# Optimization experiments

Measured on AMD Instinct MI355X. Metric: run time of the kernel, lower is better.

## Reference

```python
import jax, jax.numpy as jnp
import numpy as np

N_NODES = 100000

def sage_conv(x, edge_index, Wl, bl, Wr):
    # PyG SAGEConv: out = lin_l(mean_agg(x_src -> dst)) + lin_r(x)
    src, dst = edge_index[0], edge_index[1]
    msgs = x[src]                                   # [E, F] gather
    sums = jax.ops.segment_sum(msgs, dst, num_segments=N_NODES)   # [N, F]
    cnt = jax.ops.segment_sum(jnp.ones((edge_index.shape[1],), x.dtype), dst,
                              num_segments=N_NODES)               # [N]
    mean = sums / jnp.maximum(cnt, 1.0)[:, None]
    return mean @ Wl + bl + x @ Wr


def setup_inputs() -> dict:
    key = jax.random.key(0)
    ks = jax.random.split(key, 12)
    in_dim, hid = 32, 64
    x = jax.random.normal(ks[0], (N_NODES, in_dim), dtype=jnp.float32)
    edge_index = jax.random.randint(ks[1], (2, 3200000), 0, N_NODES)
    edge_pairs = jax.random.randint(ks[2], (1000000, 2), 0, N_NODES)
    def lin(k, fi, fo):
        bound = 1.0 / np.sqrt(fi)
        return jax.random.uniform(k, (fi, fo), jnp.float32, -bound, bound)
    params = {
        'Wl1': lin(ks[3], in_dim, hid), 'bl1': jnp.zeros((hid,), jnp.float32),
        'Wr1': lin(ks[4], in_dim, hid),
        'Wl2': lin(ks[5], hid, hid),    'bl2': jnp.zeros((hid,), jnp.float32),
        'Wr2': lin(ks[6], hid, hid),
        'Wh':  lin(ks[7], 2 * hid, 1),  'bh': jnp.zeros((1,), jnp.float32),
    }
    return dict(x=x, edge_index=edge_index, edge_pairs=edge_pairs, **params)


def reference(x, edge_index, edge_pairs, Wl1, bl1, Wr1, Wl2, bl2, Wr2, Wh, bh):
    h = jax.nn.relu(sage_conv(x, edge_index, Wl1, bl1, Wr1))
    h = jax.nn.relu(sage_conv(h, edge_index, Wl2, bl2, Wr2))
    src = h[edge_pairs[:, 0]]
    dst = h[edge_pairs[:, 1]]
    edge_repr = jnp.concatenate([src, dst], axis=1)   # [P, 2*hid]
    logits = (edge_repr @ Wh + bh)[:, 0]              # [P]
    return logits
```

## Files before the change

kernel.cpp:

```cpp
#include <hip/hip_runtime.h>

typedef unsigned int uint;
typedef unsigned short ushort;
typedef __attribute__((ext_vector_type(8))) short bf16x8;
typedef __attribute__((ext_vector_type(4))) float f32x4;

#define N_NODES 100000
#define N_EDGES 3200000
#define N_PAIRS 1000000
#define N_TILES (N_NODES / 16)

#define BUCK_SHIFT 8
#define BUCK_NODES 256
#define NBUCK ((N_NODES + BUCK_NODES - 1) / BUCK_NODES)
#define CAP 8704
#define CH 2048
#define NCHB ((N_EDGES + CH - 1) / CH)
#define EPT (CH / 256)

__device__ __forceinline__ float bf_lo(uint u) { return __uint_as_float(u << 16); }
__device__ __forceinline__ float bf_hi(uint u) { return __uint_as_float(u & 0xFFFF0000u); }
__device__ __forceinline__ ushort f2bf(float f) {
  uint u = __float_as_uint(f);
  return (ushort)((u + 0x7FFF + ((u >> 16) & 1)) >> 16);
}
__device__ __forceinline__ uint pack2bf(float lo, float hi) {
  return (uint)f2bf(lo) | ((uint)f2bf(hi) << 16);
}


__global__ void __launch_bounds__(256) k_prep(
    const float* __restrict__ x,
    const float* __restrict__ Wl1, const float* __restrict__ Wr1,
    const float* __restrict__ Wl2, const float* __restrict__ Wr2,
    ushort* __restrict__ xb, ushort* __restrict__ W1T, ushort* __restrict__ W2T,
    int* __restrict__ woff)
{
  int t = blockIdx.x * blockDim.x + threadIdx.x;
  if (t < N_NODES * 32) xb[t] = f2bf(x[t]);
  if (t < 4096) {
    int col = t >> 6, f = t & 63;
    float w = (f < 32) ? Wl1[f * 64 + col] : Wr1[(f - 32) * 64 + col];
    W1T[col * 64 + f] = f2bf(w);
  }
  if (t < 8192) {
    int col = t >> 7, f = t & 127;
    float w = (f < 64) ? Wl2[f * 64 + col] : Wr2[(f - 64) * 64 + col];
    W2T[col * 128 + f] = f2bf(w);
  }
  if (t < NBUCK) woff[t] = t * CAP;
}


__global__ void __launch_bounds__(256) k_binning(
    const int* __restrict__ src, const int* __restrict__ dst,
    int* __restrict__ woff, int* __restrict__ bucket_data)
{
  __shared__ int hist[NBUCK];
  __shared__ int rbase[NBUCK];
  int t = threadIdx.x;
  int lo = blockIdx.x * CH;
  int hi = lo + CH; if (hi > N_EDGES) hi = N_EDGES;
  for (int i = t; i < NBUCK; i += 256) hist[i] = 0;
  __syncthreads();
  int d0 = -1, d1 = -1, d2 = -1, d3 = -1, d4 = -1, d5 = -1, d6 = -1, d7 = -1;
  int s0 = 0, s1 = 0, s2 = 0, s3 = 0, s4 = 0, s5 = 0, s6 = 0, s7 = 0;
#define LOADK(k, dk, sk)                                     \
  { int e = lo + t + k * 256;                                \
    if (e < hi) { dk = dst[e]; sk = src[e];                  \
                  atomicAdd(&hist[dk >> BUCK_SHIFT], 1); } }
  LOADK(0, d0, s0) LOADK(1, d1, s1) LOADK(2, d2, s2) LOADK(3, d3, s3)
  LOADK(4, d4, s4) LOADK(5, d5, s5) LOADK(6, d6, s6) LOADK(7, d7, s7)
#undef LOADK
  __syncthreads();
  for (int i = t; i < NBUCK; i += 256) {
    int h = hist[i];
    rbase[i] = h ? atomicAdd(&woff[i], h) : 0;
    hist[i] = 0;
  }
  __syncthreads();
#define STOREK(dk, sk)                                       \
  if (dk >= 0) {                                             \
    int b = dk >> BUCK_SHIFT;                                \
    int r = atomicAdd(&hist[b], 1);                          \
    int pos = rbase[b] + r;                                  \
    if (pos < (b + 1) * CAP)                                 \
      bucket_data[pos] = (sk << BUCK_SHIFT) | (dk & (BUCK_NODES - 1)); }
  STOREK(d0, s0) STOREK(d1, s1) STOREK(d2, s2) STOREK(d3, s3)
  STOREK(d4, s4) STOREK(d5, s5) STOREK(d6, s6) STOREK(d7, s7)
#undef STOREK
}


__global__ void __launch_bounds__(512) k_bucket_csr(
    const int* __restrict__ woff, const int* __restrict__ bucket_data,
    int* __restrict__ csr, int* __restrict__ row_beg, int* __restrict__ row_end)
{
  __shared__ int hist[BUCK_NODES];
  __shared__ int sc[BUCK_NODES];
  __shared__ int offs[BUCK_NODES];
  int b = blockIdx.x;
  int t = threadIdx.x;
  int base = b * CAP;
  int cnt = woff[b] - base;
  const int* bd = bucket_data + base;
  if (t < BUCK_NODES) hist[t] = 0;
  __syncthreads();
  for (int i = t; i < cnt; i += 512) atomicAdd(&hist[bd[i] & (BUCK_NODES - 1)], 1);
  __syncthreads();
  if (t < BUCK_NODES) sc[t] = hist[t];
  __syncthreads();
  for (int off = 1; off < BUCK_NODES; off <<= 1) {
    int u = 0;
    if (t < BUCK_NODES && t >= off) u = sc[t - off];
    __syncthreads();
    if (t < BUCK_NODES) sc[t] += u;
    __syncthreads();
  }
  if (t < BUCK_NODES) {
    int start = base + sc[t] - hist[t];
    offs[t] = start;
    int node = b * BUCK_NODES + t;
    if (node < N_NODES) { row_beg[node] = start; row_end[node] = start + hist[t]; }
  }
  __syncthreads();
  for (int i = t; i < cnt; i += 512) {
    int pv = bd[i];
    int pos = atomicAdd(&offs[pv & (BUCK_NODES - 1)], 1);
    csr[pos] = pv >> BUCK_SHIFT;
  }
}


__global__ void __launch_bounds__(256) k_gather1(
    const uint4* __restrict__ xb4, const int* __restrict__ row_beg,
    const int* __restrict__ row_end, const int* __restrict__ csr,
    uint4* __restrict__ mean1)
{
  int gid = blockIdx.x * blockDim.x + threadIdx.x;
  int n = gid >> 6;
  int lane = threadIdx.x & 63;
  if (n >= N_NODES) return;
  int slot = lane >> 2;
  int fq = lane & 3;
  int beg = row_beg[n], end = row_end[n];
  int deg = end - beg;
  float s0 = 0.f, s1 = 0.f, s2 = 0.f, s3 = 0.f, s4 = 0.f, s5 = 0.f, s6 = 0.f, s7 = 0.f;
  int i = beg;
  for (; i + 31 < end; i += 32) {
    int n0 = csr[i + slot];
    int n1 = csr[i + 16 + slot];
    uint4 a = xb4[n0 * 4 + fq];
    uint4 b = xb4[n1 * 4 + fq];
    s0 += bf_lo(a.x); s1 += bf_hi(a.x); s2 += bf_lo(a.y); s3 += bf_hi(a.y);
    s4 += bf_lo(a.z); s5 += bf_hi(a.z); s6 += bf_lo(a.w); s7 += bf_hi(a.w);
    s0 += bf_lo(b.x); s1 += bf_hi(b.x); s2 += bf_lo(b.y); s3 += bf_hi(b.y);
    s4 += bf_lo(b.z); s5 += bf_hi(b.z); s6 += bf_lo(b.w); s7 += bf_hi(b.w);
  }
  for (; i < end; i += 16) {
    if (i + slot < end) {
      uint4 a = xb4[csr[i + slot] * 4 + fq];
      s0 += bf_lo(a.x); s1 += bf_hi(a.x); s2 += bf_lo(a.y); s3 += bf_hi(a.y);
      s4 += bf_lo(a.z); s5 += bf_hi(a.z); s6 += bf_lo(a.w); s7 += bf_hi(a.w);
    }
  }
#pragma unroll
  for (int off = 4; off <= 32; off <<= 1) {
    s0 += __shfl_xor(s0, off); s1 += __shfl_xor(s1, off);
    s2 += __shfl_xor(s2, off); s3 += __shfl_xor(s3, off);
    s4 += __shfl_xor(s4, off); s5 += __shfl_xor(s5, off);
    s6 += __shfl_xor(s6, off); s7 += __shfl_xor(s7, off);
  }
  if (slot == 0) {
    float invd = (deg > 0) ? 1.f / (float)deg : 0.f;
    uint4 o;
    o.x = pack2bf(s0 * invd, s1 * invd);
    o.y = pack2bf(s2 * invd, s3 * invd);
    o.z = pack2bf(s4 * invd, s5 * invd);
    o.w = pack2bf(s6 * invd, s7 * invd);
    mean1[n * 4 + fq] = o;
  }
}

__global__ void __launch_bounds__(256) k_gather2(
    const uint4* __restrict__ hb4, const int* __restrict__ row_beg,
    const int* __restrict__ row_end, const int* __restrict__ csr,
    uint4* __restrict__ mean2)
{
  int gid = blockIdx.x * blockDim.x + threadIdx.x;
  int n = gid >> 6;
  int lane = threadIdx.x & 63;
  if (n >= N_NODES) return;
  int slot = lane >> 3;
  int fq = lane & 7;
  int beg = row_beg[n], end = row_end[n];
  int deg = end - beg;
  float s0 = 0.f, s1 = 0.f, s2 = 0.f, s3 = 0.f, s4 = 0.f, s5 = 0.f, s6 = 0.f, s7 = 0.f;
  int i = beg;
  for (; i + 31 < end; i += 32) {
    int n0 = csr[i + slot];
    int n1 = csr[i + 8 + slot];
    int n2 = csr[i + 16 + slot];
    int n3 = csr[i + 24 + slot];
    uint4 a = hb4[n0 * 8 + fq];
    uint4 b = hb4[n1 * 8 + fq];
    uint4 c = hb4[n2 * 8 + fq];
    uint4 d = hb4[n3 * 8 + fq];
    s0 += bf_lo(a.x); s1 += bf_hi(a.x); s2 += bf_lo(a.y); s3 += bf_hi(a.y);
    s4 += bf_lo(a.z); s5 += bf_hi(a.z); s6 += bf_lo(a.w); s7 += bf_hi(a.w);
    s0 += bf_lo(b.x); s1 += bf_hi(b.x); s2 += bf_lo(b.y); s3 += bf_hi(b.y);
    s4 += bf_lo(b.z); s5 += bf_hi(b.z); s6 += bf_lo(b.w); s7 += bf_hi(b.w);
    s0 += bf_lo(c.x); s1 += bf_hi(c.x); s2 += bf_lo(c.y); s3 += bf_hi(c.y);
    s4 += bf_lo(c.z); s5 += bf_hi(c.z); s6 += bf_lo(c.w); s7 += bf_hi(c.w);
    s0 += bf_lo(d.x); s1 += bf_hi(d.x); s2 += bf_lo(d.y); s3 += bf_hi(d.y);
    s4 += bf_lo(d.z); s5 += bf_hi(d.z); s6 += bf_lo(d.w); s7 += bf_hi(d.w);
  }
  for (; i < end; i += 8) {
    if (i + slot < end) {
      uint4 a = hb4[csr[i + slot] * 8 + fq];
      s0 += bf_lo(a.x); s1 += bf_hi(a.x); s2 += bf_lo(a.y); s3 += bf_hi(a.y);
      s4 += bf_lo(a.z); s5 += bf_hi(a.z); s6 += bf_lo(a.w); s7 += bf_hi(a.w);
    }
  }
#pragma unroll
  for (int off = 8; off <= 32; off <<= 1) {
    s0 += __shfl_xor(s0, off); s1 += __shfl_xor(s1, off);
    s2 += __shfl_xor(s2, off); s3 += __shfl_xor(s3, off);
    s4 += __shfl_xor(s4, off); s5 += __shfl_xor(s5, off);
    s6 += __shfl_xor(s6, off); s7 += __shfl_xor(s7, off);
  }
  if (slot == 0) {
    float invd = (deg > 0) ? 1.f / (float)deg : 0.f;
    uint4 o;
    o.x = pack2bf(s0 * invd, s1 * invd);
    o.y = pack2bf(s2 * invd, s3 * invd);
    o.z = pack2bf(s4 * invd, s5 * invd);
    o.w = pack2bf(s6 * invd, s7 * invd);
    mean2[n * 8 + fq] = o;
  }
}


__global__ void __launch_bounds__(256) k_gemm1(
    const ushort* __restrict__ mean1, const ushort* __restrict__ xb,
    const ushort* __restrict__ W1T, const float* __restrict__ bl,
    ushort* __restrict__ h1b)
{
  int wave = (blockIdx.x * blockDim.x + threadIdx.x) >> 6;
  if (wave >= N_TILES) return;
  int lane = threadIdx.x & 63;
  int lc = lane & 15;
  int lg = lane >> 4;
  int n0 = wave * 16;

  bf16x8 bfr[4][2];
#pragma unroll
  for (int j = 0; j < 4; ++j)
#pragma unroll
    for (int kk = 0; kk < 2; ++kk)
      bfr[j][kk] = *(const bf16x8*)(W1T + (j * 16 + lc) * 64 + kk * 32 + lg * 8);

  f32x4 c[4];
#pragma unroll
  for (int j = 0; j < 4; ++j) {
    float b = bl[j * 16 + lc];
    c[j][0] = b; c[j][1] = b; c[j][2] = b; c[j][3] = b;
  }

  bf16x8 a0 = *(const bf16x8*)(mean1 + (n0 + lc) * 32 + lg * 8);
  bf16x8 a1 = *(const bf16x8*)(xb    + (n0 + lc) * 32 + lg * 8);
#pragma unroll
  for (int j = 0; j < 4; ++j) {
    c[j] = __builtin_amdgcn_mfma_f32_16x16x32_bf16(a0, bfr[j][0], c[j], 0, 0, 0);
    c[j] = __builtin_amdgcn_mfma_f32_16x16x32_bf16(a1, bfr[j][1], c[j], 0, 0, 0);
  }

#pragma unroll
  for (int j = 0; j < 4; ++j)
#pragma unroll
    for (int r = 0; r < 4; ++r) {
      int node = n0 + lg * 4 + r;
      h1b[node * 64 + j * 16 + lc] = f2bf(fmaxf(c[j][r], 0.f));
    }
}

__global__ void __launch_bounds__(256) k_gemm2(
    const ushort* __restrict__ mean2, const ushort* __restrict__ h1b,
    const ushort* __restrict__ W2T, const float* __restrict__ bl,
    const float* __restrict__ Wh, float* __restrict__ u, float* __restrict__ v)
{
  int wave = (blockIdx.x * blockDim.x + threadIdx.x) >> 6;
  if (wave >= N_TILES) return;
  int lane = threadIdx.x & 63;
  int lc = lane & 15;
  int lg = lane >> 4;
  int n0 = wave * 16;

  bf16x8 bfr[4][4];
#pragma unroll
  for (int j = 0; j < 4; ++j)
#pragma unroll
    for (int kk = 0; kk < 4; ++kk)
      bfr[j][kk] = *(const bf16x8*)(W2T + (j * 16 + lc) * 128 + kk * 32 + lg * 8);

  f32x4 c[4];
#pragma unroll
  for (int j = 0; j < 4; ++j) {
    float b = bl[j * 16 + lc];
    c[j][0] = b; c[j][1] = b; c[j][2] = b; c[j][3] = b;
  }

  bf16x8 a0 = *(const bf16x8*)(mean2 + (n0 + lc) * 64 + lg * 8);
  bf16x8 a1 = *(const bf16x8*)(mean2 + (n0 + lc) * 64 + 32 + lg * 8);
  bf16x8 a2 = *(const bf16x8*)(h1b   + (n0 + lc) * 64 + lg * 8);
  bf16x8 a3 = *(const bf16x8*)(h1b   + (n0 + lc) * 64 + 32 + lg * 8);
#pragma unroll
  for (int j = 0; j < 4; ++j) {
    c[j] = __builtin_amdgcn_mfma_f32_16x16x32_bf16(a0, bfr[j][0], c[j], 0, 0, 0);
    c[j] = __builtin_amdgcn_mfma_f32_16x16x32_bf16(a1, bfr[j][1], c[j], 0, 0, 0);
    c[j] = __builtin_amdgcn_mfma_f32_16x16x32_bf16(a2, bfr[j][2], c[j], 0, 0, 0);
    c[j] = __builtin_amdgcn_mfma_f32_16x16x32_bf16(a3, bfr[j][3], c[j], 0, 0, 0);
  }

  float pu0 = 0.f, pu1 = 0.f, pu2 = 0.f, pu3 = 0.f;
  float pv0 = 0.f, pv1 = 0.f, pv2 = 0.f, pv3 = 0.f;
#pragma unroll
  for (int j = 0; j < 4; ++j) {
    float wu = Wh[j * 16 + lc];
    float wv = Wh[64 + j * 16 + lc];
    float r0 = fmaxf(c[j][0], 0.f), r1 = fmaxf(c[j][1], 0.f);
    float r2 = fmaxf(c[j][2], 0.f), r3 = fmaxf(c[j][3], 0.f);
    pu0 = fmaf(r0, wu, pu0); pv0 = fmaf(r0, wv, pv0);
    pu1 = fmaf(r1, wu, pu1); pv1 = fmaf(r1, wv, pv1);
    pu2 = fmaf(r2, wu, pu2); pv2 = fmaf(r2, wv, pv2);
    pu3 = fmaf(r3, wu, pu3); pv3 = fmaf(r3, wv, pv3);
  }
#pragma unroll
  for (int off = 1; off <= 8; off <<= 1) {
    pu0 += __shfl_xor(pu0, off); pv0 += __shfl_xor(pv0, off);
    pu1 += __shfl_xor(pu1, off); pv1 += __shfl_xor(pv1, off);
    pu2 += __shfl_xor(pu2, off); pv2 += __shfl_xor(pv2, off);
    pu3 += __shfl_xor(pu3, off); pv3 += __shfl_xor(pv3, off);
  }
  if (lc == 0) {
    int node = n0 + lg * 4;
    u[node]     = pu0; v[node]     = pv0;
    u[node + 1] = pu1; v[node + 1] = pv1;
    u[node + 2] = pu2; v[node + 2] = pv2;
    u[node + 3] = pu3; v[node + 3] = pv3;
  }
}


__global__ void __launch_bounds__(256) k_edge_lite(
    const int2* __restrict__ pairs, const float* __restrict__ u,
    const float* __restrict__ v, const float* __restrict__ bh,
    float* __restrict__ out)
{
  int e = blockIdx.x * blockDim.x + threadIdx.x;
  if (e < N_PAIRS) {
    int2 pr = pairs[e];
    out[e] = u[pr.x] + v[pr.y] + bh[0];
  }
}


extern "C" void kernel_launch(void* const* d_in, const int* in_sizes, int n_in,
                              void* d_out, int out_size, void* d_ws, size_t ws_size,
                              hipStream_t stream)
{
  const float* x   = (const float*)d_in[0];
  const int*   ei  = (const int*)d_in[1];
  const int* pairs = (const int*)d_in[2];
  const float* Wl1 = (const float*)d_in[3];
  const float* bl1 = (const float*)d_in[4];
  const float* Wr1 = (const float*)d_in[5];
  const float* Wl2 = (const float*)d_in[6];
  const float* bl2 = (const float*)d_in[7];
  const float* Wr2 = (const float*)d_in[8];
  const float* Wh  = (const float*)d_in[9];
  const float* bh  = (const float*)d_in[10];
  float* out = (float*)d_out;

  const int* src = ei;
  const int* dst = ei + N_EDGES;

  char* p = (char*)d_ws;
  auto alloc = [&](size_t bytes) {
    char* r = p;
    p += (bytes + 255) & ~(size_t)255;
    return r;
  };
  int*    woff        = (int*)alloc((size_t)NBUCK * 4);
  int*    bucket_data = (int*)alloc((size_t)NBUCK * CAP * 4);
  int*    csr         = (int*)alloc((size_t)NBUCK * CAP * 4);
  int*    row_beg     = (int*)alloc((size_t)N_NODES * 4);
  int*    row_end     = (int*)alloc((size_t)N_NODES * 4);
  ushort* xb          = (ushort*)alloc((size_t)N_NODES * 32 * 2);
  ushort* mean1       = (ushort*)alloc((size_t)N_NODES * 32 * 2);
  ushort* h1b         = (ushort*)alloc((size_t)N_NODES * 64 * 2);
  ushort* W1T         = (ushort*)alloc(64 * 64 * 2);
  ushort* W2T         = (ushort*)alloc(64 * 128 * 2);
  float*  uu          = (float*)alloc((size_t)N_NODES * 4);
  float*  vv          = (float*)alloc((size_t)N_NODES * 4);
  ushort* mean2       = (ushort*)bucket_data;

  k_prep<<<(N_NODES * 32) / 256, 256, 0, stream>>>(
      x, Wl1, Wr1, Wl2, Wr2, xb, W1T, W2T, woff);
  k_binning<<<NCHB, 256, 0, stream>>>(src, dst, woff, bucket_data);
  k_bucket_csr<<<NBUCK, 512, 0, stream>>>(woff, bucket_data, csr, row_beg, row_end);

  k_gather1<<<(N_NODES * 64) / 256, 256, 0, stream>>>(
      (const uint4*)xb, row_beg, row_end, csr, (uint4*)mean1);
  k_gemm1<<<(N_TILES * 64 + 255) / 256, 256, 0, stream>>>(mean1, xb, W1T, bl1, h1b);
  k_gather2<<<(N_NODES * 64) / 256, 256, 0, stream>>>(
      (const uint4*)h1b, row_beg, row_end, csr, (uint4*)mean2);
  k_gemm2<<<(N_TILES * 64 + 255) / 256, 256, 0, stream>>>(
      mean2, h1b, W2T, bl2, Wh, uu, vv);
  k_edge_lite<<<(N_PAIRS + 255) / 256, 256, 0, stream>>>(
      (const int2*)pairs, uu, vv, bh, out);
}
```

Baseline: 231.3 us.

## Split bucket write counters into per-partition sub-buckets and vectorize x conversion

Each destination bucket's global write cursor is split into eight sub-bucket counters chosen by block index, which spreads out contention on the global atomics used in binning. The CSR builder then walks all eight sub-regions per bucket. Separately, the fp32-to-bf16 conversion of x now handles four floats per thread with vector loads and stores, so the prep kernel launches a quarter as many threads. Per-sub-bucket capacity (1216) is tighter than before, which adds a risk of silently dropping edges if one partition overflows.

New measurement: 241.1 us. 1.04x slower.

```diff
diff --git a/kernel.cpp b/kernel.cpp
--- a/kernel.cpp
+++ b/kernel.cpp
@@ -14,9 +14,10 @@
 #define BUCK_NODES 256
 #define NBUCK ((N_NODES + BUCK_NODES - 1) / BUCK_NODES)
 #define CAP 8704
+#define NPART 8
+#define CAP_SUB 1216
 #define CH 2048
 #define NCHB ((N_EDGES + CH - 1) / CH)
-#define EPT (CH / 256)
 
 __device__ __forceinline__ float bf_lo(uint u) { return __uint_as_float(u << 16); }
 __device__ __forceinline__ float bf_hi(uint u) { return __uint_as_float(u & 0xFFFF0000u); }
@@ -37,7 +38,13 @@
     int* __restrict__ woff)
 {
   int t = blockIdx.x * blockDim.x + threadIdx.x;
-  if (t < N_NODES * 32) xb[t] = f2bf(x[t]);
+  if (t < N_NODES * 8) {
+    float4 f = ((const float4*)x)[t];
+    uint2 o;
+    o.x = pack2bf(f.x, f.y);
+    o.y = pack2bf(f.z, f.w);
+    ((uint2*)xb)[t] = o;
+  }
   if (t < 4096) {
     int col = t >> 6, f = t & 63;
     float w = (f < 32) ? Wl1[f * 64 + col] : Wr1[(f - 32) * 64 + col];
@@ -48,7 +55,7 @@
     float w = (f < 64) ? Wl2[f * 64 + col] : Wr2[(f - 64) * 64 + col];
     W2T[col * 128 + f] = f2bf(w);
   }
-  if (t < NBUCK) woff[t] = t * CAP;
+  if (t < NBUCK * NPART) woff[t] = t * CAP_SUB;
 }
 
 
@@ -59,6 +66,7 @@
   __shared__ int hist[NBUCK];
   __shared__ int rbase[NBUCK];
   int t = threadIdx.x;
+  int part = blockIdx.x & (NPART - 1);
   int lo = blockIdx.x * CH;
   int hi = lo + CH; if (hi > N_EDGES) hi = N_EDGES;
   for (int i = t; i < NBUCK; i += 256) hist[i] = 0;
@@ -75,7 +83,7 @@
   __syncthreads();
   for (int i = t; i < NBUCK; i += 256) {
     int h = hist[i];
-    rbase[i] = h ? atomicAdd(&woff[i], h) : 0;
+    rbase[i] = h ? atomicAdd(&woff[i * NPART + part], h) : 0;
     hist[i] = 0;
   }
   __syncthreads();
@@ -84,7 +92,7 @@
     int b = dk >> BUCK_SHIFT;                                \
     int r = atomicAdd(&hist[b], 1);                          \
     int pos = rbase[b] + r;                                  \
-    if (pos < (b + 1) * CAP)                                 \
+    if (pos < (b * NPART + part + 1) * CAP_SUB)              \
       bucket_data[pos] = (sk << BUCK_SHIFT) | (dk & (BUCK_NODES - 1)); }
   STOREK(d0, s0) STOREK(d1, s1) STOREK(d2, s2) STOREK(d3, s3)
   STOREK(d4, s4) STOREK(d5, s5) STOREK(d6, s6) STOREK(d7, s7)
@@ -101,12 +109,16 @@
   __shared__ int offs[BUCK_NODES];
   int b = blockIdx.x;
   int t = threadIdx.x;
-  int base = b * CAP;
-  int cnt = woff[b] - base;
-  const int* bd = bucket_data + base;
   if (t < BUCK_NODES) hist[t] = 0;
   __syncthreads();
-  for (int i = t; i < cnt; i += 512) atomicAdd(&hist[bd[i] & (BUCK_NODES - 1)], 1);
+#pragma unroll
+  for (int p = 0; p < NPART; ++p) {
+    int cell = b * NPART + p;
+    int cbase = cell * CAP_SUB;
+    int cnt = woff[cell] - cbase;
+    const int* bd = bucket_data + cbase;
+    for (int i = t; i < cnt; i += 512) atomicAdd(&hist[bd[i] & (BUCK_NODES - 1)], 1);
+  }
   __syncthreads();
   if (t < BUCK_NODES) sc[t] = hist[t];
   __syncthreads();
@@ -118,16 +130,23 @@
     __syncthreads();
   }
   if (t < BUCK_NODES) {
-    int start = base + sc[t] - hist[t];
+    int start = b * CAP + sc[t] - hist[t];
     offs[t] = start;
     int node = b * BUCK_NODES + t;
     if (node < N_NODES) { row_beg[node] = start; row_end[node] = start + hist[t]; }
   }
   __syncthreads();
-  for (int i = t; i < cnt; i += 512) {
-    int pv = bd[i];
-    int pos = atomicAdd(&offs[pv & (BUCK_NODES - 1)], 1);
-    csr[pos] = pv >> BUCK_SHIFT;
+#pragma unroll
+  for (int p = 0; p < NPART; ++p) {
+    int cell = b * NPART + p;
+    int cbase = cell * CAP_SUB;
+    int cnt = woff[cell] - cbase;
+    const int* bd = bucket_data + cbase;
+    for (int i = t; i < cnt; i += 512) {
+      int pv = bd[i];
+      int pos = atomicAdd(&offs[pv & (BUCK_NODES - 1)], 1);
+      csr[pos] = pv >> BUCK_SHIFT;
+    }
   }
 }
 
@@ -391,8 +410,8 @@
     p += (bytes + 255) & ~(size_t)255;
     return r;
   };
-  int*    woff        = (int*)alloc((size_t)NBUCK * 4);
-  int*    bucket_data = (int*)alloc((size_t)NBUCK * CAP * 4);
+  int*    woff        = (int*)alloc((size_t)NBUCK * NPART * 4);
+  int*    bucket_data = (int*)alloc((size_t)NBUCK * NPART * CAP_SUB * 4);
   int*    csr         = (int*)alloc((size_t)NBUCK * CAP * 4);
   int*    row_beg     = (int*)alloc((size_t)N_NODES * 4);
   int*    row_end     = (int*)alloc((size_t)N_NODES * 4);
@@ -405,7 +424,7 @@
   float*  vv          = (float*)alloc((size_t)N_NODES * 4);
   ushort* mean2       = (ushort*)bucket_data;
 
-  k_prep<<<(N_NODES * 32) / 256, 256, 0, stream>>>(
+  k_prep<<<(N_NODES * 8 + 255) / 256, 256, 0, stream>>>(
       x, Wl1, Wr1, Wl2, Wr2, xb, W1T, W2T, woff);
   k_binning<<<NCHB, 256, 0, stream>>>(src, dst, woff, bucket_data);
   k_bucket_csr<<<NBUCK, 512, 0, stream>>>(woff, bucket_data, csr, row_beg, row_end);
```
